# Optimization experiments

Hardware: AMD Instinct MI355X
Metric: run time of the kernel (lower is better)

## Reference

```python
import jax, jax.numpy as jnp
import numpy as np

USER = 100000
ITEM = 100000
N = USER + ITEM          # total nodes
D = 64                   # latdim
DEG = 16                 # avg edges per user (before symmetrization)
L_GNN = 2                # args.gnn_layer
L_MLP = 2                # args.layer_mlp
EPS = 1e-5               # LayerNorm eps


def setup_inputs() -> dict:
    key = jax.random.key(0)
    k1, k2, k3, k4, k5 = jax.random.split(key, 5)
    # bipartite user->item edges, then symmetrize (bi_adj over N x N nodes)
    u = jax.random.randint(k1, (USER * DEG,), 0, USER)
    v = jax.random.randint(k2, (USER * DEG,), 0, ITEM) + USER
    rows = jnp.concatenate([u, v]).astype(jnp.int64)
    cols = jnp.concatenate([v, u]).astype(jnp.int64)
    # symmetric D^-1/2 A D^-1/2 normalization (matches _normalize_adj)
    deg = jnp.zeros((N,), jnp.float32).at[rows].add(1.0)
    vals = 1.0 / (jnp.sqrt(deg[rows]) * jnp.sqrt(deg[cols]))
    # xavier-uniform-ish initial embeddings (detached in the source)
    bound = float(np.sqrt(6.0 / (N + D)))
    ini_embeds = jax.random.uniform(k3, (N, D), jnp.float32, -bound, bound)
    # MLP params: L_MLP stacked Linear(latdim, latdim)
    wb = float(np.sqrt(6.0 / (D + D)))
    Ws = jax.random.uniform(k4, (L_MLP, D, D), jnp.float32, -wb, wb)
    bs = jnp.zeros((L_MLP, D), jnp.float32)
    gamma = jnp.ones((D,), jnp.float32)
    beta = jnp.zeros((D,), jnp.float32)
    return {"rows": rows, "cols": cols, "vals": vals, "ini_embeds": ini_embeds,
            "Ws": Ws, "bs": bs, "gamma": gamma, "beta": beta}


def reference(rows, cols, vals, ini_embeds, Ws, bs, gamma, beta):
    # UntrainedGCN.forward: multi-hop spmm propagation (concat=0, symetric=True)
    e = ini_embeds
    for _ in range(L_GNN):
        # spmm: out[r] += vals * e[c] for each edge (r, c)
        e = jax.ops.segment_sum(vals[:, None] * e[cols], rows, num_segments=N)
    # residual MLP: relu(Wx+b) + x per FeedForwardLayer
    for i in range(L_MLP):
        e = jax.nn.relu(e @ Ws[i].T + bs[i]) + e
    # LayerNorm over last dim
    mu = e.mean(-1, keepdims=True)
    xc = e - mu
    var = (xc * xc).mean(-1, keepdims=True)
    e = xc * jax.lax.rsqrt(var + EPS) * gamma + beta
    return e[:USER], e[USER:]
```

## Files before the change

kernel.cpp:

```cpp
#include <hip/hip_runtime.h>
#include <hip/hip_bf16.h>

#define NN      200000
#define D       64
#define NTILE   12500
#define BKT_SH  8
#define BKT_RW  256
#define NBKT    782
#define NCHUNK  256
#define L2CAP   6656
#define CPAD    16
#define RSENT   256

typedef __attribute__((ext_vector_type(8))) short short8;
typedef __attribute__((ext_vector_type(4))) short short4v;
typedef __attribute__((ext_vector_type(4))) float f32x4;

__device__ inline unsigned short f32_to_bf16_rne(float x) {
    unsigned u = __float_as_uint(x);
    unsigned r = u + 0x7FFFu + ((u >> 16) & 1u);
    return (unsigned short)(r >> 16);
}
__device__ inline float bf16_bits_to_f32(unsigned short h) {
    return __uint_as_float(((unsigned)h) << 16);
}
__device__ inline unsigned pack2_bf16_rne(float lo, float hi) {
    unsigned a = __float_as_uint(lo);
    unsigned b = __float_as_uint(hi);
    a = a + 0x7FFFu + ((a >> 16) & 1u);
    b = b + 0x7FFFu + ((b >> 16) & 1u);
    return (a >> 16) | (b & 0xFFFF0000u);
}
__device__ inline float bf_lo(unsigned u) { return __uint_as_float(u << 16); }
__device__ inline float bf_hi(unsigned u) { return __uint_as_float(u & 0xFFFF0000u); }

__global__ __launch_bounds__(256) void zero_f4(float4* __restrict__ p, int n4) {
    int i = blockIdx.x * blockDim.x + threadIdx.x;
    if (i < n4) p[i] = make_float4(0.f, 0.f, 0.f, 0.f);
}
__global__ __launch_bounds__(256) void zero_i(int* __restrict__ p, int n) {
    int i = blockIdx.x * blockDim.x + threadIdx.x;
    if (i < n) p[i] = 0;
}
__global__ __launch_bounds__(256) void cvt_bf16(const float2* __restrict__ in,
                                                unsigned* __restrict__ out, int n) {
    int stride = gridDim.x * blockDim.x;
    for (int i = blockIdx.x * blockDim.x + threadIdx.x; i < n; i += stride) {
        float2 v = in[i];
        out[i] = pack2_bf16_rne(v.x, v.y);
    }
}

template <int ALIGN>
__global__ __launch_bounds__(1024) void bkt_count(const int* __restrict__ rows,
                                                  int* __restrict__ tot_p,
                                                  int E, int epb) {
    __shared__ int h[NBKT];
    int t = threadIdx.x;
    for (int i = t; i < NBKT; i += 1024) h[i] = 0;
    __syncthreads();
    int start = blockIdx.x * epb;
    int end   = min(E, start + epb);
    for (int e = start + t; e < end; e += 1024)
        atomicAdd(&h[rows[e] >> BKT_SH], 1);
    __syncthreads();
    for (int i = t; i < NBKT; i += 1024) {
        int c   = h[i];
        int res = (c + ALIGN - 1) & ~(ALIGN - 1);
        if (res) atomicAdd(&tot_p[i * CPAD], res);
    }
}

__global__ __launch_bounds__(1024) void bkt_scan(const int* __restrict__ tot_p,
                                                 int* __restrict__ bktstart,
                                                 int* __restrict__ cursor_p) {
    __shared__ int s[1024];
    int t = threadIdx.x;
    int v = (t < NBKT) ? tot_p[t * CPAD] : 0;
    s[t] = v;
    __syncthreads();
    #pragma unroll
    for (int d = 1; d < 1024; d <<= 1) {
        int a = (t >= d) ? s[t - d] : 0;
        __syncthreads();
        s[t] += a;
        __syncthreads();
    }
    if (t < NBKT) {
        int ex = s[t] - v;
        bktstart[t] = ex;
        cursor_p[t * CPAD] = ex;
    }
    if (t == 0) bktstart[NBKT] = s[1023];
}

template <int ALIGN>
__global__ __launch_bounds__(1024) void scatter_l1(const int* __restrict__ rows,
                                                   const int* __restrict__ cols,
                                                   const float* __restrict__ vals,
                                                   int* __restrict__ cursor_p,
                                                   int2* __restrict__ packed,
                                                   int E, int epb) {
    __shared__ int h[NBKT];
    __shared__ int base[NBKT];
    int t = threadIdx.x;
    for (int i = t; i < NBKT; i += 1024) h[i] = 0;
    __syncthreads();
    int start = blockIdx.x * epb;
    int end   = min(E, start + epb);
    for (int e = start + t; e < end; e += 1024)
        atomicAdd(&h[rows[e] >> BKT_SH], 1);
    __syncthreads();
    for (int i = t; i < NBKT; i += 1024) {
        int c   = h[i];
        int res = (c + ALIGN - 1) & ~(ALIGN - 1);
        int b0  = res ? atomicAdd(&cursor_p[i * CPAD], res) : 0;
        base[i] = b0;
        for (int j = c; j < res; ++j)
            packed[b0 + j] = make_int2(RSENT << 18, 0);
        h[i] = 0;
    }
    __syncthreads();
    for (int e = start + t; e < end; e += 1024) {
        int r = rows[e];
        int b = r >> BKT_SH;
        int p = base[b] + atomicAdd(&h[b], 1);
        packed[p] = make_int2(cols[e] | ((r & (BKT_RW - 1)) << 18),
                              __float_as_int(vals[e]));
    }
}

__global__ __launch_bounds__(256) void sort_l2(const int* __restrict__ bktstart,
                                               int2* __restrict__ packed,
                                               int* __restrict__ rp,
                                               int* __restrict__ rpe) {
    __shared__ int2 sm[L2CAP];
    __shared__ int  cnt[BKT_RW];
    __shared__ int  cur[BKT_RW];
    int b = blockIdx.x;
    int s = bktstart[b];
    int e = bktstart[b + 1];
    int n = e - s;
    if (n > L2CAP) n = L2CAP;
    int t = threadIdx.x;
    cnt[t] = 0;
    __syncthreads();
    for (int i = t; i < n; i += 256) {
        int2 v = packed[s + i];
        sm[i] = v;
        int r = (v.x >> 18) & 0x1FF;
        if (r < BKT_RW) atomicAdd(&cnt[r], 1);
    }
    __syncthreads();
    #pragma unroll
    for (int d = 1; d < BKT_RW; d <<= 1) {
        int a = (t >= d) ? cnt[t - d] : 0;
        __syncthreads();
        cnt[t] += a;
        __syncthreads();
    }
    {
        int ex = t ? cnt[t - 1] : 0;
        cur[t] = ex;
        int g = (b << BKT_SH) + t;
        if (g < NN) { rp[g] = s + ex; rpe[g] = s + cnt[t]; }
    }
    __syncthreads();
    for (int i = t; i < n; i += 256) {
        int2 v = sm[i];
        int  r = (v.x >> 18) & 0x1FF;
        if (r < BKT_RW) {
            int p = atomicAdd(&cur[r], 1);
            packed[s + p] = make_int2(v.x & 0x3FFFF, v.y);
        }
    }
}

template <int OUT_BF16>
__global__ __launch_bounds__(256) void spmm_q(const int* __restrict__ rp,
                                              const int* __restrict__ rpe,
                                              const int2* __restrict__ packed,
                                              const uint2* __restrict__ ein,
                                              uint2* __restrict__ out_bf,
                                              float4* __restrict__ out_f32, int n) {
    int wave = (blockIdx.x * 256 + threadIdx.x) >> 6;
    int lane = threadIdx.x & 63;
    int l    = lane & 15;
    int row  = wave * 4 + (lane >> 4);

    float ax = 0.f, ay = 0.f, az = 0.f, aw = 0.f;
    int s = 0, e = 0;
    if (row < n) { s = rp[row]; e = rpe[row]; }

    for (int base = s; base < e; base += 16) {
        int cnt = e - base; if (cnt > 16) cnt = 16;
        int2 ev = make_int2(0, 0);
        if (l < cnt) ev = packed[base + l];
        int k = 0;
        for (; k + 4 <= cnt; k += 4) {
            int   c0 = __shfl(ev.x, k,     16), c1 = __shfl(ev.x, k + 1, 16);
            int   c2 = __shfl(ev.x, k + 2, 16), c3 = __shfl(ev.x, k + 3, 16);
            float v0 = __int_as_float(__shfl(ev.y, k,     16));
            float v1 = __int_as_float(__shfl(ev.y, k + 1, 16));
            float v2 = __int_as_float(__shfl(ev.y, k + 2, 16));
            float v3 = __int_as_float(__shfl(ev.y, k + 3, 16));
            uint2 g0 = ein[c0 * 16 + l];
            uint2 g1 = ein[c1 * 16 + l];
            uint2 g2 = ein[c2 * 16 + l];
            uint2 g3 = ein[c3 * 16 + l];
            ax += v0 * bf_lo(g0.x); ay += v0 * bf_hi(g0.x);
            az += v0 * bf_lo(g0.y); aw += v0 * bf_hi(g0.y);
            ax += v1 * bf_lo(g1.x); ay += v1 * bf_hi(g1.x);
            az += v1 * bf_lo(g1.y); aw += v1 * bf_hi(g1.y);
            ax += v2 * bf_lo(g2.x); ay += v2 * bf_hi(g2.x);
            az += v2 * bf_lo(g2.y); aw += v2 * bf_hi(g2.y);
            ax += v3 * bf_lo(g3.x); ay += v3 * bf_hi(g3.x);
            az += v3 * bf_lo(g3.y); aw += v3 * bf_hi(g3.y);
        }
        for (; k + 2 <= cnt; k += 2) {
            int   c0 = __shfl(ev.x, k, 16), c1 = __shfl(ev.x, k + 1, 16);
            float v0 = __int_as_float(__shfl(ev.y, k,     16));
            float v1 = __int_as_float(__shfl(ev.y, k + 1, 16));
            uint2 g0 = ein[c0 * 16 + l];
            uint2 g1 = ein[c1 * 16 + l];
            ax += v0 * bf_lo(g0.x); ay += v0 * bf_hi(g0.x);
            az += v0 * bf_lo(g0.y); aw += v0 * bf_hi(g0.y);
            ax += v1 * bf_lo(g1.x); ay += v1 * bf_hi(g1.x);
            az += v1 * bf_lo(g1.y); aw += v1 * bf_hi(g1.y);
        }
        if (k < cnt) {
            int   c0 = __shfl(ev.x, k, 16);
            float v0 = __int_as_float(__shfl(ev.y, k, 16));
            uint2 g0 = ein[c0 * 16 + l];
            ax += v0 * bf_lo(g0.x); ay += v0 * bf_hi(g0.x);
            az += v0 * bf_lo(g0.y); aw += v0 * bf_hi(g0.y);
        }
    }
    if (row < n) {
        if (OUT_BF16) {
            out_bf[(size_t)row * 16 + l] =
                make_uint2(pack2_bf16_rne(ax, ay), pack2_bf16_rne(az, aw));
        } else {
            out_f32[(size_t)row * 16 + l] = make_float4(ax, ay, az, aw);
        }
    }
}

__global__ __launch_bounds__(256) void spmm_scatter(const int* __restrict__ rows,
                                                    const int* __restrict__ cols,
                                                    const float* __restrict__ vals,
                                                    const float* __restrict__ ein,
                                                    float* __restrict__ eout, int E) {
    int gid  = blockIdx.x * blockDim.x + threadIdx.x;
    int wid  = gid >> 6;
    int lane = threadIdx.x & 63;
    int nw   = (gridDim.x * blockDim.x) >> 6;
    for (int e = wid; e < E; e += nw) {
        int   r = rows[e];
        int   c = cols[e];
        float v = vals[e];
        float x = ein[(size_t)c * D + lane];
        unsafeAtomicAdd(&eout[(size_t)r * D + lane], v * x);
    }
}

__global__ __launch_bounds__(256) void mlp_v2(float* __restrict__ e,
                                              const float* __restrict__ Ws,
                                              const float* __restrict__ bs,
                                              const float* __restrict__ gamma,
                                              const float* __restrict__ beta) {
    __shared__ unsigned short wlds[2][64][72];
    __shared__ float tb[4][16][68];

    int t    = threadIdx.x;
    int wv   = t >> 6;
    int lane = t & 63;
    int fr   = t & 15;
    int fq   = lane >> 4;

    for (int i = t * 4; i < 2 * 64 * 64; i += 1024) {
        float4 f = *(const float4*)(Ws + i);
        int l = i >> 12, r = (i >> 6) & 63, c = i & 63;
        short4v s4;
        s4[0] = (short)f32_to_bf16_rne(f.x);
        s4[1] = (short)f32_to_bf16_rne(f.y);
        s4[2] = (short)f32_to_bf16_rne(f.z);
        s4[3] = (short)f32_to_bf16_rne(f.w);
        *(short4v*)&wlds[l][r][c] = s4;
    }
    __syncthreads();

    float bia[2][4], gam[4], bet[4];
    #pragma unroll
    for (int nt = 0; nt < 4; ++nt) {
        bia[0][nt] = bs[nt * 16 + fr];
        bia[1][nt] = bs[64 + nt * 16 + fr];
        gam[nt]    = gamma[nt * 16 + fr];
        bet[nt]    = beta[nt * 16 + fr];
    }

    float (*tw)[68] = tb[wv];

    for (int tile = blockIdx.x * 4 + wv; tile < NTILE; tile += gridDim.x * 4) {
        float* base = e + (size_t)tile * 1024;

        #pragma unroll
        for (int it = 0; it < 4; ++it) {
            int idx = it * 256 + lane * 4;
            *(float4*)&tw[idx >> 6][idx & 63] = *(const float4*)(base + idx);
        }

        #pragma unroll
        for (int l = 0; l < 2; ++l) {
            short8 xh[2], xl[2];
            #pragma unroll
            for (int kk = 0; kk < 2; ++kk) {
                const float* s = &tw[fr][kk * 32 + fq * 8];
                float4 a = *(const float4*)s;
                float4 b4 = *(const float4*)(s + 4);
                float v[8] = {a.x, a.y, a.z, a.w, b4.x, b4.y, b4.z, b4.w};
                #pragma unroll
                for (int j = 0; j < 8; ++j) {
                    unsigned short hh = f32_to_bf16_rne(v[j]);
                    xh[kk][j] = (short)hh;
                    xl[kk][j] = (short)f32_to_bf16_rne(v[j] - bf16_bits_to_f32(hh));
                }
            }
            f32x4 acc[4];
            #pragma unroll
            for (int nt = 0; nt < 4; ++nt) {
                float bb = bia[l][nt];
                acc[nt] = f32x4{bb, bb, bb, bb};
                #pragma unroll
                for (int kk = 0; kk < 2; ++kk) {
                    short8 w8 = *(const short8*)&wlds[l][nt * 16 + fr][kk * 32 + fq * 8];
                    acc[nt] = __builtin_amdgcn_mfma_f32_16x16x32_bf16(xl[kk], w8, acc[nt], 0, 0, 0);
                    acc[nt] = __builtin_amdgcn_mfma_f32_16x16x32_bf16(xh[kk], w8, acc[nt], 0, 0, 0);
                }
            }
            #pragma unroll
            for (int nt = 0; nt < 4; ++nt)
                #pragma unroll
                for (int j = 0; j < 4; ++j) {
                    float* cell = &tw[fq * 4 + j][nt * 16 + fr];
                    *cell = fmaxf(acc[nt][j], 0.f) + *cell;
                }
        }

        float y2[4][4], sm[4], sq[4];
        #pragma unroll
        for (int j = 0; j < 4; ++j) { sm[j] = 0.f; sq[j] = 0.f; }
        #pragma unroll
        for (int nt = 0; nt < 4; ++nt)
            #pragma unroll
            for (int j = 0; j < 4; ++j) {
                float v = tw[fq * 4 + j][nt * 16 + fr];
                y2[nt][j] = v;
                sm[j] += v; sq[j] += v * v;
            }
        #pragma unroll
        for (int off = 1; off < 16; off <<= 1) {
            #pragma unroll
            for (int j = 0; j < 4; ++j) {
                sm[j] += __shfl_xor(sm[j], off);
                sq[j] += __shfl_xor(sq[j], off);
            }
        }
        #pragma unroll
        for (int j = 0; j < 4; ++j) {
            float mu  = sm[j] * (1.f / 64.f);
            float var = sq[j] * (1.f / 64.f) - mu * mu;
            float rs  = rsqrtf(var + 1e-5f);
            #pragma unroll
            for (int nt = 0; nt < 4; ++nt)
                tw[fq * 4 + j][nt * 16 + fr] = (y2[nt][j] - mu) * rs * gam[nt] + bet[nt];
        }

        #pragma unroll
        for (int it = 0; it < 4; ++it) {
            int idx = it * 256 + lane * 4;
            *(float4*)(base + idx) = *(const float4*)&tw[idx >> 6][idx & 63];
        }
    }
}

template <int ALIGN>
static void run_csr(const int* rows, const int* cols, const float* vals,
                    const float* ini, float* out, char* w, int E, size_t packed_cap,
                    hipStream_t stream) {
    size_t inibf_b  = (size_t)NN * 32 * 4;
    size_t e1bf_b   = inibf_b;
    size_t packed_b = packed_cap * 8;
    size_t rp_b     = (((size_t)NN + 1) * 4 + 63) & ~(size_t)63;
    size_t rpe_b    = (ALIGN > 1) ? rp_b : 0;
    size_t bsrt_b   = (((size_t)NBKT + 1) * 4 + 63) & ~(size_t)63;
    size_t pad_b    = (size_t)NBKT * CPAD * 4;

    unsigned* ini_bf   = (unsigned*)w;  w += inibf_b;
    unsigned* e1_bf    = (unsigned*)w;  w += e1bf_b;
    int2*     packed   = (int2*)w;      w += packed_b;
    int*      rp       = (int*)w;       w += rp_b;
    int*      rpe      = (ALIGN > 1) ? (int*)w : rp + 1;  w += rpe_b;
    int*      bktstart = (int*)w;       w += bsrt_b;
    int*      tot_p    = (int*)w;       w += pad_b;
    int*      cursor_p = (int*)w;

    int epb = (E + NCHUNK - 1) / NCHUNK;
    cvt_bf16<<<2048, 256, 0, stream>>>((const float2*)ini, ini_bf, NN * 32);
    zero_i<<<(NBKT * CPAD + 255) / 256, 256, 0, stream>>>(tot_p, NBKT * CPAD);
    bkt_count<ALIGN><<<NCHUNK, 1024, 0, stream>>>(rows, tot_p, E, epb);
    bkt_scan<<<1, 1024, 0, stream>>>(tot_p, bktstart, cursor_p);
    scatter_l1<ALIGN><<<NCHUNK, 1024, 0, stream>>>(rows, cols, vals, cursor_p, packed, E, epb);
    sort_l2<<<NBKT, 256, 0, stream>>>(bktstart, packed, rp, rpe);

    int waves = (NN + 3) / 4;
    int blocks = (waves + 3) / 4;
    spmm_q<1><<<blocks, 256, 0, stream>>>(rp, rpe, packed, (const uint2*)ini_bf,
                                          (uint2*)e1_bf, nullptr, NN);
    spmm_q<0><<<blocks, 256, 0, stream>>>(rp, rpe, packed, (const uint2*)e1_bf,
                                          nullptr, (float4*)out, NN);
}

extern "C" void kernel_launch(void* const* d_in, const int* in_sizes, int n_in,
                              void* d_out, int out_size, void* d_ws, size_t ws_size,
                              hipStream_t stream) {
    const int*   rows  = (const int*)d_in[0];
    const int*   cols  = (const int*)d_in[1];
    const float* vals  = (const float*)d_in[2];
    const float* ini   = (const float*)d_in[3];
    const float* Ws    = (const float*)d_in[4];
    const float* bs    = (const float*)d_in[5];
    const float* gamma = (const float*)d_in[6];
    const float* beta  = (const float*)d_in[7];
    float* out = (float*)d_out;
    int E = in_sizes[0];

    size_t inibf_b = (size_t)NN * 32 * 4;
    size_t rp_b    = (((size_t)NN + 1) * 4 + 63) & ~(size_t)63;
    size_t bsrt_b  = (((size_t)NBKT + 1) * 4 + 63) & ~(size_t)63;
    size_t pad_b   = (size_t)NBKT * CPAD * 4;
    size_t cap8    = (size_t)E + (size_t)NBKT * NCHUNK * 7;
    size_t cap1    = (size_t)E;
    size_t need8   = 2 * inibf_b + cap8 * 8 + 2 * rp_b + bsrt_b + 2 * pad_b;
    size_t need1   = 2 * inibf_b + cap1 * 8 + rp_b + bsrt_b + 2 * pad_b;

    if (ws_size >= need8) {
        run_csr<8>(rows, cols, vals, ini, out, (char*)d_ws, E, cap8, stream);
    } else if (ws_size >= need1) {
        run_csr<1>(rows, cols, vals, ini, out, (char*)d_ws, E, cap1, stream);
    } else {
        float* e1 = (float*)d_ws;
        int n4 = out_size / 4;
        int zb = (n4 + 255) / 256;
        zero_f4<<<zb, 256, 0, stream>>>((float4*)e1,  n4);
        zero_f4<<<zb, 256, 0, stream>>>((float4*)out, n4);
        spmm_scatter<<<12800, 256, 0, stream>>>(rows, cols, vals, ini, e1, E);
        spmm_scatter<<<12800, 256, 0, stream>>>(rows, cols, vals, e1, out, E);
    }

    mlp_v2<<<512, 256, 0, stream>>>(out, Ws, bs, gamma, beta);
}
```

Measured before the change: 234.0 us.

## Fuse second SpMM hop with residual MLP and LayerNorm epilogue

The second gather-SpMM now writes its 16-row tile into shared memory, and one wave runs the two-layer MFMA residual MLP and LayerNorm on it before storing the final output. The separate mlp_v2 pass, with its fp32 write and re-read of the full embedding matrix, is dropped on the CSR paths. In exchange, every block converts both weight matrices to bf16 in LDS, and only one of four waves does the MLP, so the epilogue is serialised per block and the weight-load cost is repeated across 12500 blocks.

```diff
diff --git a/kernel.cpp b/kernel.cpp
--- a/kernel.cpp
+++ b/kernel.cpp
@@ -176,72 +176,177 @@
     }
 }
 
-template <int OUT_BF16>
-__global__ __launch_bounds__(256) void spmm_q(const int* __restrict__ rp,
-                                              const int* __restrict__ rpe,
-                                              const int2* __restrict__ packed,
-                                              const uint2* __restrict__ ein,
-                                              uint2* __restrict__ out_bf,
-                                              float4* __restrict__ out_f32, int n) {
+#define GATHER_BODY(rpv, rpev, packedv, einv)                                      \
+    float ax = 0.f, ay = 0.f, az = 0.f, aw = 0.f;                                  \
+    {                                                                              \
+        int s_ = rpv, e_ = rpev;                                                   \
+        for (int base_ = s_; base_ < e_; base_ += 16) {                            \
+            int cnt = e_ - base_; if (cnt > 16) cnt = 16;                          \
+            int2 ev = make_int2(0, 0);                                             \
+            if (l < cnt) ev = packedv[base_ + l];                                  \
+            int k = 0;                                                             \
+            for (; k + 4 <= cnt; k += 4) {                                         \
+                int   c0 = __shfl(ev.x, k,     16), c1 = __shfl(ev.x, k + 1, 16);  \
+                int   c2 = __shfl(ev.x, k + 2, 16), c3 = __shfl(ev.x, k + 3, 16);  \
+                float v0 = __int_as_float(__shfl(ev.y, k,     16));                \
+                float v1 = __int_as_float(__shfl(ev.y, k + 1, 16));                \
+                float v2 = __int_as_float(__shfl(ev.y, k + 2, 16));                \
+                float v3 = __int_as_float(__shfl(ev.y, k + 3, 16));                \
+                uint2 g0 = einv[c0 * 16 + l];                                      \
+                uint2 g1 = einv[c1 * 16 + l];                                      \
+                uint2 g2 = einv[c2 * 16 + l];                                      \
+                uint2 g3 = einv[c3 * 16 + l];                                      \
+                ax += v0 * bf_lo(g0.x); ay += v0 * bf_hi(g0.x);                    \
+                az += v0 * bf_lo(g0.y); aw += v0 * bf_hi(g0.y);                    \
+                ax += v1 * bf_lo(g1.x); ay += v1 * bf_hi(g1.x);                    \
+                az += v1 * bf_lo(g1.y); aw += v1 * bf_hi(g1.y);                    \
+                ax += v2 * bf_lo(g2.x); ay += v2 * bf_hi(g2.x);                    \
+                az += v2 * bf_lo(g2.y); aw += v2 * bf_hi(g2.y);                    \
+                ax += v3 * bf_lo(g3.x); ay += v3 * bf_hi(g3.x);                    \
+                az += v3 * bf_lo(g3.y); aw += v3 * bf_hi(g3.y);                    \
+            }                                                                      \
+            for (; k < cnt; ++k) {                                                 \
+                int   c0 = __shfl(ev.x, k, 16);                                    \
+                float v0 = __int_as_float(__shfl(ev.y, k, 16));                    \
+                uint2 g0 = einv[c0 * 16 + l];                                      \
+                ax += v0 * bf_lo(g0.x); ay += v0 * bf_hi(g0.x);                    \
+                az += v0 * bf_lo(g0.y); aw += v0 * bf_hi(g0.y);                    \
+            }                                                                      \
+        }                                                                          \
+    }
+
+__global__ __launch_bounds__(256) void spmm_q1(const int* __restrict__ rp,
+                                               const int* __restrict__ rpe,
+                                               const int2* __restrict__ packed,
+                                               const uint2* __restrict__ ein,
+                                               uint2* __restrict__ out_bf, int n) {
     int wave = (blockIdx.x * 256 + threadIdx.x) >> 6;
     int lane = threadIdx.x & 63;
     int l    = lane & 15;
     int row  = wave * 4 + (lane >> 4);
-
-    float ax = 0.f, ay = 0.f, az = 0.f, aw = 0.f;
-    int s = 0, e = 0;
-    if (row < n) { s = rp[row]; e = rpe[row]; }
-
-    for (int base = s; base < e; base += 16) {
-        int cnt = e - base; if (cnt > 16) cnt = 16;
-        int2 ev = make_int2(0, 0);
-        if (l < cnt) ev = packed[base + l];
-        int k = 0;
-        for (; k + 4 <= cnt; k += 4) {
-            int   c0 = __shfl(ev.x, k,     16), c1 = __shfl(ev.x, k + 1, 16);
-            int   c2 = __shfl(ev.x, k + 2, 16), c3 = __shfl(ev.x, k + 3, 16);
-            float v0 = __int_as_float(__shfl(ev.y, k,     16));
-            float v1 = __int_as_float(__shfl(ev.y, k + 1, 16));
-            float v2 = __int_as_float(__shfl(ev.y, k + 2, 16));
-            float v3 = __int_as_float(__shfl(ev.y, k + 3, 16));
-            uint2 g0 = ein[c0 * 16 + l];
-            uint2 g1 = ein[c1 * 16 + l];
-            uint2 g2 = ein[c2 * 16 + l];
-            uint2 g3 = ein[c3 * 16 + l];
-            ax += v0 * bf_lo(g0.x); ay += v0 * bf_hi(g0.x);
-            az += v0 * bf_lo(g0.y); aw += v0 * bf_hi(g0.y);
-            ax += v1 * bf_lo(g1.x); ay += v1 * bf_hi(g1.x);
-            az += v1 * bf_lo(g1.y); aw += v1 * bf_hi(g1.y);
-            ax += v2 * bf_lo(g2.x); ay += v2 * bf_hi(g2.x);
-            az += v2 * bf_lo(g2.y); aw += v2 * bf_hi(g2.y);
-            ax += v3 * bf_lo(g3.x); ay += v3 * bf_hi(g3.x);
-            az += v3 * bf_lo(g3.y); aw += v3 * bf_hi(g3.y);
-        }
-        for (; k + 2 <= cnt; k += 2) {
-            int   c0 = __shfl(ev.x, k, 16), c1 = __shfl(ev.x, k + 1, 16);
-            float v0 = __int_as_float(__shfl(ev.y, k,     16));
-            float v1 = __int_as_float(__shfl(ev.y, k + 1, 16));
-            uint2 g0 = ein[c0 * 16 + l];
-            uint2 g1 = ein[c1 * 16 + l];
-            ax += v0 * bf_lo(g0.x); ay += v0 * bf_hi(g0.x);
-            az += v0 * bf_lo(g0.y); aw += v0 * bf_hi(g0.y);
-            ax += v1 * bf_lo(g1.x); ay += v1 * bf_hi(g1.x);
-            az += v1 * bf_lo(g1.y); aw += v1 * bf_hi(g1.y);
-        }
-        if (k < cnt) {
-            int   c0 = __shfl(ev.x, k, 16);
-            float v0 = __int_as_float(__shfl(ev.y, k, 16));
-            uint2 g0 = ein[c0 * 16 + l];
-            ax += v0 * bf_lo(g0.x); ay += v0 * bf_hi(g0.x);
-            az += v0 * bf_lo(g0.y); aw += v0 * bf_hi(g0.y);
-        }
-    }
-    if (row < n) {
-        if (OUT_BF16) {
-            out_bf[(size_t)row * 16 + l] =
-                make_uint2(pack2_bf16_rne(ax, ay), pack2_bf16_rne(az, aw));
-        } else {
-            out_f32[(size_t)row * 16 + l] = make_float4(ax, ay, az, aw);
+    if (row >= n) return;
+    GATHER_BODY(rp[row], rpe[row], packed, ein)
+    out_bf[(size_t)row * 16 + l] = make_uint2(pack2_bf16_rne(ax, ay), pack2_bf16_rne(az, aw));
+}
+
+__global__ __launch_bounds__(256) void spmm_mlp(const int* __restrict__ rp,
+                                                const int* __restrict__ rpe,
+                                                const int2* __restrict__ packed,
+                                                const uint2* __restrict__ ein,
+                                                float* __restrict__ out,
+                                                const float* __restrict__ Ws,
+                                                const float* __restrict__ bs,
+                                                const float* __restrict__ gamma,
+                                                const float* __restrict__ beta) {
+    __shared__ unsigned short wlds[2][64][72];
+    __shared__ float tb[16][68];
+
+    int t    = threadIdx.x;
+    int lane = t & 63;
+    int wv   = t >> 6;
+    int l    = lane & 15;
+    int q    = lane >> 4;
+
+    for (int i = t * 4; i < 2 * 64 * 64; i += 1024) {
+        float4 f = *(const float4*)(Ws + i);
+        int ly = i >> 12, r = (i >> 6) & 63, c = i & 63;
+        short4v s4;
+        s4[0] = (short)f32_to_bf16_rne(f.x);
+        s4[1] = (short)f32_to_bf16_rne(f.y);
+        s4[2] = (short)f32_to_bf16_rne(f.z);
+        s4[3] = (short)f32_to_bf16_rne(f.w);
+        *(short4v*)&wlds[ly][r][c] = s4;
+    }
+
+    int row_local = wv * 4 + q;
+    int row = blockIdx.x * 16 + row_local;
+    GATHER_BODY(rp[row], rpe[row], packed, ein)
+    *(float4*)&tb[row_local][l * 4] = make_float4(ax, ay, az, aw);
+    __syncthreads();
+
+    if (wv == 0) {
+        int fr = lane & 15;
+        int fq = lane >> 4;
+        float bia[2][4], gam[4], bet[4];
+        #pragma unroll
+        for (int nt = 0; nt < 4; ++nt) {
+            bia[0][nt] = bs[nt * 16 + fr];
+            bia[1][nt] = bs[64 + nt * 16 + fr];
+            gam[nt]    = gamma[nt * 16 + fr];
+            bet[nt]    = beta[nt * 16 + fr];
+        }
+
+        #pragma unroll
+        for (int ly = 0; ly < 2; ++ly) {
+            short8 xh[2], xl[2];
+            #pragma unroll
+            for (int kk = 0; kk < 2; ++kk) {
+                const float* s = &tb[fr][kk * 32 + fq * 8];
+                float4 a = *(const float4*)s;
+                float4 b4 = *(const float4*)(s + 4);
+                float v[8] = {a.x, a.y, a.z, a.w, b4.x, b4.y, b4.z, b4.w};
+                #pragma unroll
+                for (int j = 0; j < 8; ++j) {
+                    unsigned short hh = f32_to_bf16_rne(v[j]);
+                    xh[kk][j] = (short)hh;
+                    xl[kk][j] = (short)f32_to_bf16_rne(v[j] - bf16_bits_to_f32(hh));
+                }
+            }
+            f32x4 acc[4];
+            #pragma unroll
+            for (int nt = 0; nt < 4; ++nt) {
+                float bb = bia[ly][nt];
+                acc[nt] = f32x4{bb, bb, bb, bb};
+                #pragma unroll
+                for (int kk = 0; kk < 2; ++kk) {
+                    short8 w8 = *(const short8*)&wlds[ly][nt * 16 + fr][kk * 32 + fq * 8];
+                    acc[nt] = __builtin_amdgcn_mfma_f32_16x16x32_bf16(xl[kk], w8, acc[nt], 0, 0, 0);
+                    acc[nt] = __builtin_amdgcn_mfma_f32_16x16x32_bf16(xh[kk], w8, acc[nt], 0, 0, 0);
+                }
+            }
+            #pragma unroll
+            for (int nt = 0; nt < 4; ++nt)
+                #pragma unroll
+                for (int j = 0; j < 4; ++j) {
+                    float* cell = &tb[fq * 4 + j][nt * 16 + fr];
+                    *cell = fmaxf(acc[nt][j], 0.f) + *cell;
+                }
+        }
+
+        float y2[4][4], sm[4], sq[4];
+        #pragma unroll
+        for (int j = 0; j < 4; ++j) { sm[j] = 0.f; sq[j] = 0.f; }
+        #pragma unroll
+        for (int nt = 0; nt < 4; ++nt)
+            #pragma unroll
+            for (int j = 0; j < 4; ++j) {
+                float v = tb[fq * 4 + j][nt * 16 + fr];
+                y2[nt][j] = v;
+                sm[j] += v; sq[j] += v * v;
+            }
+        #pragma unroll
+        for (int off = 1; off < 16; off <<= 1) {
+            #pragma unroll
+            for (int j = 0; j < 4; ++j) {
+                sm[j] += __shfl_xor(sm[j], off);
+                sq[j] += __shfl_xor(sq[j], off);
+            }
+        }
+        #pragma unroll
+        for (int j = 0; j < 4; ++j) {
+            float mu  = sm[j] * (1.f / 64.f);
+            float var = sq[j] * (1.f / 64.f) - mu * mu;
+            float rs  = rsqrtf(var + 1e-5f);
+            #pragma unroll
+            for (int nt = 0; nt < 4; ++nt)
+                tb[fq * 4 + j][nt * 16 + fr] = (y2[nt][j] - mu) * rs * gam[nt] + bet[nt];
+        }
+
+        float* base = out + (size_t)blockIdx.x * 1024;
+        #pragma unroll
+        for (int it = 0; it < 4; ++it) {
+            int idx = it * 256 + lane * 4;
+            *(float4*)(base + idx) = *(const float4*)&tb[idx >> 6][idx & 63];
         }
     }
 }
@@ -303,13 +408,11 @@
 
     for (int tile = blockIdx.x * 4 + wv; tile < NTILE; tile += gridDim.x * 4) {
         float* base = e + (size_t)tile * 1024;
-
         #pragma unroll
         for (int it = 0; it < 4; ++it) {
             int idx = it * 256 + lane * 4;
             *(float4*)&tw[idx >> 6][idx & 63] = *(const float4*)(base + idx);
         }
-
         #pragma unroll
         for (int l = 0; l < 2; ++l) {
             short8 xh[2], xl[2];
@@ -346,7 +449,6 @@
                     *cell = fmaxf(acc[nt][j], 0.f) + *cell;
                 }
         }
-
         float y2[4][4], sm[4], sq[4];
         #pragma unroll
         for (int j = 0; j < 4; ++j) { sm[j] = 0.f; sq[j] = 0.f; }
@@ -375,7 +477,6 @@
             for (int nt = 0; nt < 4; ++nt)
                 tw[fq * 4 + j][nt * 16 + fr] = (y2[nt][j] - mu) * rs * gam[nt] + bet[nt];
         }
-
         #pragma unroll
         for (int it = 0; it < 4; ++it) {
             int idx = it * 256 + lane * 4;
@@ -387,7 +488,8 @@
 template <int ALIGN>
 static void run_csr(const int* rows, const int* cols, const float* vals,
                     const float* ini, float* out, char* w, int E, size_t packed_cap,
-                    hipStream_t stream) {
+                    const float* Ws, const float* bs, const float* gamma,
+                    const float* beta, hipStream_t stream) {
     size_t inibf_b  = (size_t)NN * 32 * 4;
     size_t e1bf_b   = inibf_b;
     size_t packed_b = packed_cap * 8;
@@ -413,12 +515,10 @@
     scatter_l1<ALIGN><<<NCHUNK, 1024, 0, stream>>>(rows, cols, vals, cursor_p, packed, E, epb);
     sort_l2<<<NBKT, 256, 0, stream>>>(bktstart, packed, rp, rpe);
 
-    int waves = (NN + 3) / 4;
-    int blocks = (waves + 3) / 4;
-    spmm_q<1><<<blocks, 256, 0, stream>>>(rp, rpe, packed, (const uint2*)ini_bf,
-                                          (uint2*)e1_bf, nullptr, NN);
-    spmm_q<0><<<blocks, 256, 0, stream>>>(rp, rpe, packed, (const uint2*)e1_bf,
-                                          nullptr, (float4*)out, NN);
+    spmm_q1<<<NTILE, 256, 0, stream>>>(rp, rpe, packed, (const uint2*)ini_bf,
+                                       (uint2*)e1_bf, NN);
+    spmm_mlp<<<NTILE, 256, 0, stream>>>(rp, rpe, packed, (const uint2*)e1_bf,
+                                        out, Ws, bs, gamma, beta);
 }
 
 extern "C" void kernel_launch(void* const* d_in, const int* in_sizes, int n_in,
@@ -445,9 +545,11 @@
     size_t need1   = 2 * inibf_b + cap1 * 8 + rp_b + bsrt_b + 2 * pad_b;
 
     if (ws_size >= need8) {
-        run_csr<8>(rows, cols, vals, ini, out, (char*)d_ws, E, cap8, stream);
+        run_csr<8>(rows, cols, vals, ini, out, (char*)d_ws, E, cap8,
+                   Ws, bs, gamma, beta, stream);
     } else if (ws_size >= need1) {
-        run_csr<1>(rows, cols, vals, ini, out, (char*)d_ws, E, cap1, stream);
+        run_csr<1>(rows, cols, vals, ini, out, (char*)d_ws, E, cap1,
+                   Ws, bs, gamma, beta, stream);
     } else {
         float* e1 = (float*)d_ws;
         int n4 = out_size / 4;
@@ -456,7 +558,6 @@
         zero_f4<<<zb, 256, 0, stream>>>((float4*)out, n4);
         spmm_scatter<<<12800, 256, 0, stream>>>(rows, cols, vals, ini, e1, E);
         spmm_scatter<<<12800, 256, 0, stream>>>(rows, cols, vals, e1, out, E);
-    }
-
-    mlp_v2<<<512, 256, 0, stream>>>(out, Ws, bs, gamma, beta);
-}
+        mlp_v2<<<512, 256, 0, stream>>>(out, Ws, bs, gamma, beta);
+    }
+}
```

Result: slower. 257.2 us (+9.9%).

## Store second SpMM output as bf16 and feed MLP bf16 input directly

Applied to the files above, without the earlier changes.

The second SpMM hop now writes bf16 into a reused buffer instead of fp32 to the output, and the MLP reads that bf16 tile, skipping the low-part MFMA on the first layer because the input is exactly bf16. The bucket sort's chunk count becomes a runtime parameter, with 512 chunks used when workspace allows, and the L2 capacity is raised. MLP grid size doubles. This cuts global traffic between SpMM and MLP at the cost of rounding the layer-two activations to bf16, which may affect accuracy.

```diff
diff --git a/kernel.cpp b/kernel.cpp
--- a/kernel.cpp
+++ b/kernel.cpp
@@ -7,8 +7,7 @@
 #define BKT_SH  8
 #define BKT_RW  256
 #define NBKT    782
-#define NCHUNK  256
-#define L2CAP   6656
+#define L2CAP   7680
 #define CPAD    16
 #define RSENT   256
 
@@ -176,22 +175,19 @@
     }
 }
 
-template <int OUT_BF16>
-__global__ __launch_bounds__(256) void spmm_q(const int* __restrict__ rp,
+__global__ __launch_bounds__(256) void spmm_g(const int* __restrict__ rp,
                                               const int* __restrict__ rpe,
                                               const int2* __restrict__ packed,
                                               const uint2* __restrict__ ein,
-                                              uint2* __restrict__ out_bf,
-                                              float4* __restrict__ out_f32, int n) {
+                                              uint2* __restrict__ out_bf, int n) {
     int wave = (blockIdx.x * 256 + threadIdx.x) >> 6;
     int lane = threadIdx.x & 63;
     int l    = lane & 15;
     int row  = wave * 4 + (lane >> 4);
+    if (row >= n) return;
 
     float ax = 0.f, ay = 0.f, az = 0.f, aw = 0.f;
-    int s = 0, e = 0;
-    if (row < n) { s = rp[row]; e = rpe[row]; }
-
+    int s = rp[row], e = rpe[row];
     for (int base = s; base < e; base += 16) {
         int cnt = e - base; if (cnt > 16) cnt = 16;
         int2 ev = make_int2(0, 0);
@@ -217,18 +213,7 @@
             ax += v3 * bf_lo(g3.x); ay += v3 * bf_hi(g3.x);
             az += v3 * bf_lo(g3.y); aw += v3 * bf_hi(g3.y);
         }
-        for (; k + 2 <= cnt; k += 2) {
-            int   c0 = __shfl(ev.x, k, 16), c1 = __shfl(ev.x, k + 1, 16);
-            float v0 = __int_as_float(__shfl(ev.y, k,     16));
-            float v1 = __int_as_float(__shfl(ev.y, k + 1, 16));
-            uint2 g0 = ein[c0 * 16 + l];
-            uint2 g1 = ein[c1 * 16 + l];
-            ax += v0 * bf_lo(g0.x); ay += v0 * bf_hi(g0.x);
-            az += v0 * bf_lo(g0.y); aw += v0 * bf_hi(g0.y);
-            ax += v1 * bf_lo(g1.x); ay += v1 * bf_hi(g1.x);
-            az += v1 * bf_lo(g1.y); aw += v1 * bf_hi(g1.y);
-        }
-        if (k < cnt) {
+        for (; k < cnt; ++k) {
             int   c0 = __shfl(ev.x, k, 16);
             float v0 = __int_as_float(__shfl(ev.y, k, 16));
             uint2 g0 = ein[c0 * 16 + l];
@@ -236,14 +221,7 @@
             az += v0 * bf_lo(g0.y); aw += v0 * bf_hi(g0.y);
         }
     }
-    if (row < n) {
-        if (OUT_BF16) {
-            out_bf[(size_t)row * 16 + l] =
-                make_uint2(pack2_bf16_rne(ax, ay), pack2_bf16_rne(az, aw));
-        } else {
-            out_f32[(size_t)row * 16 + l] = make_float4(ax, ay, az, aw);
-        }
-    }
+    out_bf[(size_t)row * 16 + l] = make_uint2(pack2_bf16_rne(ax, ay), pack2_bf16_rne(az, aw));
 }
 
 __global__ __launch_bounds__(256) void spmm_scatter(const int* __restrict__ rows,
@@ -264,7 +242,9 @@
     }
 }
 
-__global__ __launch_bounds__(256) void mlp_v2(float* __restrict__ e,
+template <int IN_BF16>
+__global__ __launch_bounds__(256) void mlp_v2(const uint2* __restrict__ in_bf,
+                                              float* __restrict__ out,
                                               const float* __restrict__ Ws,
                                               const float* __restrict__ bs,
                                               const float* __restrict__ gamma,
@@ -302,12 +282,26 @@
     float (*tw)[68] = tb[wv];
 
     for (int tile = blockIdx.x * 4 + wv; tile < NTILE; tile += gridDim.x * 4) {
-        float* base = e + (size_t)tile * 1024;
-
-        #pragma unroll
-        for (int it = 0; it < 4; ++it) {
-            int idx = it * 256 + lane * 4;
-            *(float4*)&tw[idx >> 6][idx & 63] = *(const float4*)(base + idx);
+        float* baseo = out + (size_t)tile * 1024;
+
+        if (IN_BF16) {
+            const uint2* bi = in_bf + (size_t)tile * 256;
+            #pragma unroll
+            for (int it = 0; it < 4; ++it) {
+                int idx = it * 64 + lane;
+                uint2 u = bi[idx];
+                int r = idx >> 4, c = (idx & 15) * 4;
+                tw[r][c]     = bf_lo(u.x);
+                tw[r][c + 1] = bf_hi(u.x);
+                tw[r][c + 2] = bf_lo(u.y);
+                tw[r][c + 3] = bf_hi(u.y);
+            }
+        } else {
+            #pragma unroll
+            for (int it = 0; it < 4; ++it) {
+                int idx = it * 256 + lane * 4;
+                *(float4*)&tw[idx >> 6][idx & 63] = *(const float4*)(baseo + idx);
+            }
         }
 
         #pragma unroll
@@ -334,7 +328,8 @@
                 #pragma unroll
                 for (int kk = 0; kk < 2; ++kk) {
                     short8 w8 = *(const short8*)&wlds[l][nt * 16 + fr][kk * 32 + fq * 8];
-                    acc[nt] = __builtin_amdgcn_mfma_f32_16x16x32_bf16(xl[kk], w8, acc[nt], 0, 0, 0);
+                    if (!(IN_BF16 && l == 0))
+                        acc[nt] = __builtin_amdgcn_mfma_f32_16x16x32_bf16(xl[kk], w8, acc[nt], 0, 0, 0);
                     acc[nt] = __builtin_amdgcn_mfma_f32_16x16x32_bf16(xh[kk], w8, acc[nt], 0, 0, 0);
                 }
             }
@@ -379,7 +374,7 @@
         #pragma unroll
         for (int it = 0; it < 4; ++it) {
             int idx = it * 256 + lane * 4;
-            *(float4*)(base + idx) = *(const float4*)&tw[idx >> 6][idx & 63];
+            *(float4*)(baseo + idx) = *(const float4*)&tw[idx >> 6][idx & 63];
         }
     }
 }
@@ -387,7 +382,8 @@
 template <int ALIGN>
 static void run_csr(const int* rows, const int* cols, const float* vals,
                     const float* ini, float* out, char* w, int E, size_t packed_cap,
-                    hipStream_t stream) {
+                    int nchunk, const float* Ws, const float* bs,
+                    const float* gamma, const float* beta, hipStream_t stream) {
     size_t inibf_b  = (size_t)NN * 32 * 4;
     size_t e1bf_b   = inibf_b;
     size_t packed_b = packed_cap * 8;
@@ -405,20 +401,19 @@
     int*      tot_p    = (int*)w;       w += pad_b;
     int*      cursor_p = (int*)w;
 
-    int epb = (E + NCHUNK - 1) / NCHUNK;
+    int epb = (E + nchunk - 1) / nchunk;
     cvt_bf16<<<2048, 256, 0, stream>>>((const float2*)ini, ini_bf, NN * 32);
     zero_i<<<(NBKT * CPAD + 255) / 256, 256, 0, stream>>>(tot_p, NBKT * CPAD);
-    bkt_count<ALIGN><<<NCHUNK, 1024, 0, stream>>>(rows, tot_p, E, epb);
+    bkt_count<ALIGN><<<nchunk, 1024, 0, stream>>>(rows, tot_p, E, epb);
     bkt_scan<<<1, 1024, 0, stream>>>(tot_p, bktstart, cursor_p);
-    scatter_l1<ALIGN><<<NCHUNK, 1024, 0, stream>>>(rows, cols, vals, cursor_p, packed, E, epb);
+    scatter_l1<ALIGN><<<nchunk, 1024, 0, stream>>>(rows, cols, vals, cursor_p, packed, E, epb);
     sort_l2<<<NBKT, 256, 0, stream>>>(bktstart, packed, rp, rpe);
 
-    int waves = (NN + 3) / 4;
-    int blocks = (waves + 3) / 4;
-    spmm_q<1><<<blocks, 256, 0, stream>>>(rp, rpe, packed, (const uint2*)ini_bf,
-                                          (uint2*)e1_bf, nullptr, NN);
-    spmm_q<0><<<blocks, 256, 0, stream>>>(rp, rpe, packed, (const uint2*)e1_bf,
-                                          nullptr, (float4*)out, NN);
+    spmm_g<<<NTILE, 256, 0, stream>>>(rp, rpe, packed, (const uint2*)ini_bf,
+                                      (uint2*)e1_bf, NN);
+    spmm_g<<<NTILE, 256, 0, stream>>>(rp, rpe, packed, (const uint2*)e1_bf,
+                                      (uint2*)ini_bf, NN);
+    mlp_v2<1><<<1024, 256, 0, stream>>>((const uint2*)ini_bf, out, Ws, bs, gamma, beta);
 }
 
 extern "C" void kernel_launch(void* const* d_in, const int* in_sizes, int n_in,
@@ -439,15 +434,20 @@
     size_t rp_b    = (((size_t)NN + 1) * 4 + 63) & ~(size_t)63;
     size_t bsrt_b  = (((size_t)NBKT + 1) * 4 + 63) & ~(size_t)63;
     size_t pad_b   = (size_t)NBKT * CPAD * 4;
-    size_t cap8    = (size_t)E + (size_t)NBKT * NCHUNK * 7;
-    size_t cap1    = (size_t)E;
-    size_t need8   = 2 * inibf_b + cap8 * 8 + 2 * rp_b + bsrt_b + 2 * pad_b;
-    size_t need1   = 2 * inibf_b + cap1 * 8 + rp_b + bsrt_b + 2 * pad_b;
-
-    if (ws_size >= need8) {
-        run_csr<8>(rows, cols, vals, ini, out, (char*)d_ws, E, cap8, stream);
-    } else if (ws_size >= need1) {
-        run_csr<1>(rows, cols, vals, ini, out, (char*)d_ws, E, cap1, stream);
+    auto cap  = [&](int nc) { return (size_t)E + (size_t)NBKT * nc * 7; };
+    auto need = [&](int nc, int nrp) {
+        return 2 * inibf_b + cap(nc) * 8 + (size_t)nrp * rp_b + bsrt_b + 2 * pad_b;
+    };
+
+    if (ws_size >= need(512, 2)) {
+        run_csr<8>(rows, cols, vals, ini, out, (char*)d_ws, E, cap(512), 512,
+                   Ws, bs, gamma, beta, stream);
+    } else if (ws_size >= need(256, 2)) {
+        run_csr<8>(rows, cols, vals, ini, out, (char*)d_ws, E, cap(256), 256,
+                   Ws, bs, gamma, beta, stream);
+    } else if (ws_size >= 2 * inibf_b + (size_t)E * 8 + rp_b + bsrt_b + 2 * pad_b) {
+        run_csr<1>(rows, cols, vals, ini, out, (char*)d_ws, E, (size_t)E, 256,
+                   Ws, bs, gamma, beta, stream);
     } else {
         float* e1 = (float*)d_ws;
         int n4 = out_size / 4;
@@ -456,7 +456,6 @@
         zero_f4<<<zb, 256, 0, stream>>>((float4*)out, n4);
         spmm_scatter<<<12800, 256, 0, stream>>>(rows, cols, vals, ini, e1, E);
         spmm_scatter<<<12800, 256, 0, stream>>>(rows, cols, vals, e1, out, E);
-    }
-
-    mlp_v2<<<512, 256, 0, stream>>>(out, Ws, bs, gamma, beta);
-}
+        mlp_v2<0><<<1024, 256, 0, stream>>>(nullptr, out, Ws, bs, gamma, beta);
+    }
+}
```

After: 243.7 us. 4.1% more time.
